# Performance work log

Measured on AMD Instinct MI355X. Metric: run time of the kernel, lower is better.

## Reference

```python
import jax, jax.numpy as jnp
import numpy as np
import math

B, T, C = 2, 2048, 1024
N_HEAD = 16
HEAD_DIM = C // N_HEAD


def setup_inputs() -> dict:
    key = jax.random.key(0)
    k1, k2, k3 = jax.random.split(key, 3)
    x = jax.random.normal(k1, (B, T, C), dtype=jnp.float32)
    # causal mask: positions where mask == 0 get -inf
    mask = jnp.tril(jnp.ones((T, T), dtype=bool))[None, None, :, :]
    W_attn = jax.random.normal(k2, (C, 3 * C), dtype=jnp.float32) * (1.0 / math.sqrt(C))
    b_attn = jnp.zeros((3 * C,), dtype=jnp.float32)
    W_proj = jax.random.normal(k3, (C, C), dtype=jnp.float32) * (1.0 / math.sqrt(C))
    b_proj = jnp.zeros((C,), dtype=jnp.float32)
    return {"x": x, "mask": mask, "W_attn": W_attn, "b_attn": b_attn,
            "W_proj": W_proj, "b_proj": b_proj}


def reference(x, mask, W_attn, b_attn, W_proj, b_proj):
    Bx, Tx, Cx = x.shape
    qkv = x @ W_attn + b_attn                      # [B,T,3C]
    q, k, v = jnp.split(qkv, 3, axis=2)
    # [B,T,C] -> [B,H,T,D]
    q = q.reshape(Bx, Tx, N_HEAD, HEAD_DIM).transpose(0, 2, 1, 3)
    k = k.reshape(Bx, Tx, N_HEAD, HEAD_DIM).transpose(0, 2, 1, 3)
    v = v.reshape(Bx, Tx, N_HEAD, HEAD_DIM).transpose(0, 2, 1, 3)
    scale = 1.0 / math.sqrt(HEAD_DIM)
    att = jnp.einsum('bhqd,bhkd->bhqk', q, k) * scale   # [B,H,T,T]
    att = jnp.where(mask, att, -jnp.inf)
    att = jax.nn.softmax(att, axis=-1)
    y = jnp.einsum('bhqk,bhkd->bhqd', att, v)            # [B,H,T,D]
    y = y.transpose(0, 2, 1, 3).reshape(Bx, Tx, Cx)      # [B,T,C]
    return y @ W_proj + b_proj
```

## Files before the change

### kernel.cpp

```cpp
#include <hip/hip_runtime.h>
#include <hip/hip_bf16.h>
#include <cstdint>

typedef unsigned short u16;
typedef unsigned int u32;
typedef unsigned long long u64;
using f32x4 = __attribute__((ext_vector_type(4))) float;
using s16x8 = __attribute__((ext_vector_type(8))) short;
using u32x4 = __attribute__((ext_vector_type(4))) u32;

#define NB 2
#define NT 2048
#define NC 1024
#define NH 16
#define HD 64

__device__ __forceinline__ u16 f2b(float f) {
    unsigned u = __float_as_uint(f);
    unsigned r = (u + 0x7FFFu + ((u >> 16) & 1u)) >> 16;
    return (u16)r;
}

__device__ __forceinline__ u32 cvtpk(float a, float b) {
    u32 r;
    asm("v_cvt_pk_bf16_f32 %0, %1, %2" : "=v"(r) : "v"(a), "v"(b));
    return r;
}
__device__ __forceinline__ void swap32(u32& a, u32& b) {
    asm("v_permlane32_swap_b32 %0, %1" : "+v"(a), "+v"(b));
}
__device__ __forceinline__ void swap16(u32& a, u32& b) {
    asm("v_permlane16_swap_b32 %0, %1" : "+v"(a), "+v"(b));
}

__device__ __forceinline__ void gl_lds16(const void* g, const void* l) {
    __builtin_amdgcn_global_load_lds(
        (const __attribute__((address_space(1))) unsigned int*)g,
        (__attribute__((address_space(3))) unsigned int*)l, 16, 0, 0);
}

__global__ __launch_bounds__(256) void conv_bf16(const float* __restrict__ in,
                                                 u16* __restrict__ out, int n4) {
    int i = blockIdx.x * 256 + threadIdx.x;
    if (i >= n4) return;
    float4 v = ((const float4*)in)[i];
    u64 pack = (u64)f2b(v.x) | ((u64)f2b(v.y) << 16) |
               ((u64)f2b(v.z) << 32) | ((u64)f2b(v.w) << 48);
    ((u64*)out)[i] = pack;
}

__global__ __launch_bounds__(256) void transpose_bf16(const float* __restrict__ W,
                                                      u16* __restrict__ Wt,
                                                      int K, int N) {
    __shared__ u16 s[64][65];
    const int n0 = blockIdx.x * 64, k0 = blockIdx.y * 64;
    const int t = threadIdx.x;
    const int tr = t >> 4, tc4 = (t & 15) * 4;
#pragma unroll
    for (int i = 0; i < 4; i++) {
        int r = tr + i * 16;
        float4 v = *(const float4*)&W[(size_t)(k0 + r) * N + n0 + tc4];
        s[r][tc4 + 0] = f2b(v.x);
        s[r][tc4 + 1] = f2b(v.y);
        s[r][tc4 + 2] = f2b(v.z);
        s[r][tc4 + 3] = f2b(v.w);
    }
    __syncthreads();
#pragma unroll
    for (int i = 0; i < 4; i++) {
        int nl = tr + i * 16;
        u64 pack = (u64)s[tc4 + 0][nl] | ((u64)s[tc4 + 1][nl] << 16) |
                   ((u64)s[tc4 + 2][nl] << 32) | ((u64)s[tc4 + 3][nl] << 48);
        *(u64*)&Wt[(size_t)(n0 + nl) * K + k0 + tc4] = pack;
    }
}

template <int OUT_BF16>
__global__ __launch_bounds__(256) void gemm_bt(const u16* __restrict__ A,
                                               const u16* __restrict__ Bt,
                                               const float* __restrict__ bias,
                                               void* __restrict__ Cout,
                                               int M, int N, int K) {
    __shared__ u16 As[2][128 * 32];
    __shared__ u16 Bs[2][128 * 32];
    const int tid = threadIdx.x;
    const int lane = tid & 63, w = tid >> 6;
    const int nx = gridDim.x;
    const int f = blockIdx.y * nx + blockIdx.x;
    const int qq = (nx * gridDim.y) >> 3;
    const int nid = (f & 7) * qq + (f >> 3);
    const int m0 = (nid / nx) * 128, n0 = (nid % nx) * 128;
    const int wm = w >> 1, wn = w & 1;
    f32x4 acc[4][4] = {};

    const int srow = 32 * w + (lane >> 2);
    const int scol = (lane & 3) * 8;
    const u16* aP0 = &A[(size_t)(m0 + srow) * K + scol];
    const u16* aP1 = aP0 + (size_t)16 * K;
    const u16* bP0 = &Bt[(size_t)(n0 + srow) * K + scol];
    const u16* bP1 = bP0 + (size_t)16 * K;

    auto STAGE = [&](int t) {
        const int buf = t & 1;
        const int k0 = t * 32;
        gl_lds16(aP0 + k0, &As[buf][w * 1024 + lane * 8]);
        gl_lds16(aP1 + k0, &As[buf][w * 1024 + 512 + lane * 8]);
        gl_lds16(bP0 + k0, &Bs[buf][w * 1024 + lane * 8]);
        gl_lds16(bP1 + k0, &Bs[buf][w * 1024 + 512 + lane * 8]);
    };

    const int nt = K >> 5;
    STAGE(0);
    for (int t = 0; t < nt; ++t) {
        asm volatile("s_waitcnt vmcnt(0)" ::: "memory");
        __builtin_amdgcn_s_barrier();
        if (t + 1 < nt) STAGE(t + 1);

        const u16* Asb = As[t & 1];
        const u16* Bsb = Bs[t & 1];
        s16x8 af[4], bf[4];
#pragma unroll
        for (int mt = 0; mt < 4; mt++)
            af[mt] = *(const s16x8*)&Asb[(wm * 64 + mt * 16 + (lane & 15)) * 32 + (lane >> 4) * 8];
#pragma unroll
        for (int nt2 = 0; nt2 < 4; nt2++)
            bf[nt2] = *(const s16x8*)&Bsb[(wn * 64 + nt2 * 16 + (lane & 15)) * 32 + (lane >> 4) * 8];
        __builtin_amdgcn_s_setprio(1);
#pragma unroll
        for (int mt = 0; mt < 4; mt++)
#pragma unroll
            for (int nt2 = 0; nt2 < 4; nt2++)
                acc[mt][nt2] = __builtin_amdgcn_mfma_f32_16x16x32_bf16(af[mt], bf[nt2], acc[mt][nt2], 0, 0, 0);
        __builtin_amdgcn_s_setprio(0);
    }

#pragma unroll
    for (int mt = 0; mt < 4; mt++) {
        int row = m0 + wm * 64 + mt * 16 + (lane >> 4) * 4;
#pragma unroll
        for (int nt2 = 0; nt2 < 4; nt2++) {
            int col = n0 + wn * 64 + nt2 * 16 + (lane & 15);
            float bs = bias[col];
#pragma unroll
            for (int r = 0; r < 4; r++) {
                float v = acc[mt][nt2][r] + bs;
                if (OUT_BF16)
                    ((u16*)Cout)[(size_t)(row + r) * N + col] = f2b(v);
                else
                    ((float*)Cout)[(size_t)(row + r) * N + col] = v;
            }
        }
    }
}

__global__ __launch_bounds__(256) void gemm_bt_n64(const u16* __restrict__ A,
                                                   const u16* __restrict__ Bt,
                                                   const float* __restrict__ bias,
                                                   float* __restrict__ Cout,
                                                   int M, int N, int K) {
    __shared__ u16 As[2][128 * 32];
    __shared__ u16 Bs[2][64 * 32];
    const int tid = threadIdx.x;
    const int lane = tid & 63, w = tid >> 6;
    const int nx = gridDim.x;
    const int f = blockIdx.y * nx + blockIdx.x;
    const int qq = (nx * gridDim.y) >> 3;
    const int nid = (f & 7) * qq + (f >> 3);
    const int m0 = (nid / nx) * 128, n0 = (nid % nx) * 64;
    f32x4 acc[2][4] = {};

    const int srow = 32 * w + (lane >> 2);
    const int srowB = 16 * w + (lane >> 2);
    const int scol = (lane & 3) * 8;
    const u16* aP0 = &A[(size_t)(m0 + srow) * K + scol];
    const u16* aP1 = aP0 + (size_t)16 * K;
    const u16* bP0 = &Bt[(size_t)(n0 + srowB) * K + scol];

    auto STAGE = [&](int t) {
        const int buf = t & 1;
        const int k0 = t * 32;
        gl_lds16(aP0 + k0, &As[buf][w * 1024 + lane * 8]);
        gl_lds16(aP1 + k0, &As[buf][w * 1024 + 512 + lane * 8]);
        gl_lds16(bP0 + k0, &Bs[buf][w * 512 + lane * 8]);
    };

    const int nt = K >> 5;
    STAGE(0);
    for (int t = 0; t < nt; ++t) {
        asm volatile("s_waitcnt vmcnt(0)" ::: "memory");
        __builtin_amdgcn_s_barrier();
        if (t + 1 < nt) STAGE(t + 1);

        const u16* Asb = As[t & 1];
        const u16* Bsb = Bs[t & 1];
        s16x8 af[2], bf[4];
#pragma unroll
        for (int mt = 0; mt < 2; mt++)
            af[mt] = *(const s16x8*)&Asb[(w * 32 + mt * 16 + (lane & 15)) * 32 + (lane >> 4) * 8];
#pragma unroll
        for (int nt2 = 0; nt2 < 4; nt2++)
            bf[nt2] = *(const s16x8*)&Bsb[(nt2 * 16 + (lane & 15)) * 32 + (lane >> 4) * 8];
        __builtin_amdgcn_s_setprio(1);
#pragma unroll
        for (int mt = 0; mt < 2; mt++)
#pragma unroll
            for (int nt2 = 0; nt2 < 4; nt2++)
                acc[mt][nt2] = __builtin_amdgcn_mfma_f32_16x16x32_bf16(af[mt], bf[nt2], acc[mt][nt2], 0, 0, 0);
        __builtin_amdgcn_s_setprio(0);
    }

#pragma unroll
    for (int mt = 0; mt < 2; mt++) {
        int row = m0 + w * 32 + mt * 16 + (lane >> 4) * 4;
#pragma unroll
        for (int nt2 = 0; nt2 < 4; nt2++) {
            int col = n0 + nt2 * 16 + (lane & 15);
            float bs = bias[col];
#pragma unroll
            for (int r = 0; r < 4; r++)
                Cout[(size_t)(row + r) * N + col] = acc[mt][nt2][r] + bs;
        }
    }
}

__global__ __launch_bounds__(256) void v_transpose(const u16* __restrict__ qkv,
                                                   u16* __restrict__ Vt) {
    __shared__ u16 s[64][65];
    const int t0 = blockIdx.x * 64;
    const int b = blockIdx.y >> 4, h = blockIdx.y & 15;
    const int t = threadIdx.x;
    const int tr = t >> 4, tc4 = (t & 15) * 4;
    const u16* src = qkv + (size_t)b * NT * (3 * NC) + 2 * NC + h * HD;
#pragma unroll
    for (int i = 0; i < 4; i++) {
        int r = tr + i * 16;
        u64 v = *(const u64*)&src[(size_t)(t0 + r) * (3 * NC) + tc4];
        s[r][tc4 + 0] = (u16)v;
        s[r][tc4 + 1] = (u16)(v >> 16);
        s[r][tc4 + 2] = (u16)(v >> 32);
        s[r][tc4 + 3] = (u16)(v >> 48);
    }
    __syncthreads();
    u16* dstb = Vt + (size_t)(b * NH + h) * HD * NT;
#pragma unroll
    for (int i = 0; i < 4; i++) {
        int d = tr + i * 16;
        u64 pack = (u64)s[tc4 + 0][d] | ((u64)s[tc4 + 1][d] << 16) |
                   ((u64)s[tc4 + 2][d] << 32) | ((u64)s[tc4 + 3][d] << 48);
        *(u64*)&dstb[(size_t)d * NT + t0 + tc4] = pack;
    }
}

__global__ __launch_bounds__(512) void attn_kernel(const u16* __restrict__ qkv,
                                                   const u16* __restrict__ Vt,
                                                   u16* __restrict__ yb) {
    __shared__ __align__(16) u16 Kb[2][2][64 * 64];
    __shared__ __align__(16) u16 Vb[2][2][64 * 64];

    const int l = threadIdx.x & 63;
    const int q16 = l & 15, g = l >> 4;
    const int wv = threadIdx.x >> 6;
    const int rg = wv & 3, hf = wv >> 2;
    const int i0 = blockIdx.x;
    const int xcd = i0 & 7, idx = i0 >> 3;
    const int hh = xcd * 4 + (idx >> 4);
    const int pr = idx & 15;
    const int b = hh >> 4, h = hh & 15;

    const u16* qkvb = qkv + (size_t)b * NT * (3 * NC);

    const int srow = l >> 3;
    const int sc8 = (l & 7) ^ (srow & 7);
    const u16* kSrc0 = qkvb + NC + h * HD + (size_t)(8 * rg + srow) * (3 * NC) + sc8 * 8;
    const u16* kSrc1 = kSrc0 + (size_t)32 * (3 * NC);
    const u16* vSrc0 = Vt + ((size_t)(b * NH + h) * HD + 8 * rg + srow) * NT + sc8 * 8;
    const u16* vSrc1 = vSrc0 + (size_t)32 * NT;
    const size_t kStep = (size_t)64 * (3 * NC);

    const float sc2 = 0.125f * 1.44269504088896340736f;
    const float SHIFT = 5.0f * 1.44269504088896340736f;
    const int sw = q16 & 7;

    u32 kfo[4][2], vfo[2][4];
#pragma unroll
    for (int ii = 0; ii < 4; ii++)
#pragma unroll
        for (int kc = 0; kc < 2; kc++)
            kfo[ii][kc] = (u32)(((16 * ii + q16) * 64 + ((4 * kc + g) ^ sw) * 8) * 2);
#pragma unroll
    for (int ks = 0; ks < 2; ks++)
#pragma unroll
        for (int dt = 0; dt < 4; dt++)
            vfo[ks][dt] = (u32)(((16 * dt + q16) * 64 + ((4 * ks + g) ^ sw) * 8) * 2);

#pragma unroll 1
    for (int sc = 0; sc < 2; ++sc) {
        const int cc = (sc == 0) ? (31 - pr) : pr;
        const int nt = cc + 1;
        const int h0 = (nt + 1) >> 1;
        const int base = hf ? h0 : 0;
        const int myN = hf ? (nt - h0) : h0;
        const int qw = cc * 64 + 16 * rg;

        s16x8 qf[2];
#pragma unroll
        for (int kc = 0; kc < 2; kc++)
            qf[kc] = *(const s16x8*)(qkvb + (size_t)(qw + q16) * (3 * NC) + h * HD + kc * 32 + g * 8);

        f32x4 yacc[4] = {};
        float lsum = 0.f;

        const u16* kP0 = kSrc0 + (size_t)base * kStep;
        const u16* kP1 = kSrc1 + (size_t)base * kStep;
        const u16* vP0 = vSrc0 + base * 64;
        const u16* vP1 = vSrc1 + base * 64;

        auto STAGE = [&](int buf) {
            gl_lds16(kP0, &Kb[hf][buf][rg * 512 + l * 8]);
            gl_lds16(kP1, &Kb[hf][buf][2048 + rg * 512 + l * 8]);
            gl_lds16(vP0, &Vb[hf][buf][rg * 512 + l * 8]);
            gl_lds16(vP1, &Vb[hf][buf][2048 + rg * 512 + l * 8]);
            kP0 += kStep; kP1 += kStep; vP0 += 64; vP1 += 64;
        };

        if (myN > 0) STAGE(base & 1);
        for (int u = 0; u < h0; ++u) {
            const int t = base + u;
            const bool act = (u < myN);
            asm volatile("s_waitcnt vmcnt(0)" ::: "memory");
            __builtin_amdgcn_s_barrier();
            if (u + 1 < myN) STAGE((t + 1) & 1);

            if (act) {
                const char* Kc = (const char*)&Kb[hf][t & 1][0];
                const char* Vc = (const char*)&Vb[hf][t & 1][0];

                s16x8 kf[4][2];
#pragma unroll
                for (int ii = 0; ii < 4; ii++)
#pragma unroll
                    for (int kc = 0; kc < 2; kc++)
                        kf[ii][kc] = *(const s16x8*)(Kc + kfo[ii][kc]);

                s16x8 vf0[4];
#pragma unroll
                for (int dt = 0; dt < 4; dt++)
                    vf0[dt] = *(const s16x8*)(Vc + vfo[0][dt]);

                f32x4 sacc[4] = {};
                __builtin_amdgcn_s_setprio(1);
#pragma unroll
                for (int ii = 0; ii < 4; ii++)
#pragma unroll
                    for (int kc = 0; kc < 2; kc++)
                        sacc[ii] = __builtin_amdgcn_mfma_f32_16x16x32_bf16(kf[ii][kc], qf[kc], sacc[ii], 0, 0, 0);
                __builtin_amdgcn_s_setprio(0);

                if (t == cc) {
                    const int kv0 = t * 64;
#pragma unroll
                    for (int ii = 0; ii < 4; ii++)
#pragma unroll
                        for (int r = 0; r < 4; r++)
                            if (kv0 + 16 * ii + 4 * g + r > qw + q16) sacc[ii][r] = -1e30f;
                }

                float p[4][4];
                float ps = 0.f;
#pragma unroll
                for (int ii = 0; ii < 4; ii++)
#pragma unroll
                    for (int r = 0; r < 4; r++) {
                        p[ii][r] = exp2f(fmaf(sacc[ii][r], sc2, -SHIFT));
                        ps += p[ii][r];
                    }
                lsum += ps;

                s16x8 pfrag[2];
#pragma unroll
                for (int ks = 0; ks < 2; ks++) {
                    u32 C0 = cvtpk(p[2 * ks][0], p[2 * ks][1]);
                    u32 C1 = cvtpk(p[2 * ks][2], p[2 * ks][3]);
                    u32 D0 = cvtpk(p[2 * ks + 1][0], p[2 * ks + 1][1]);
                    u32 D1 = cvtpk(p[2 * ks + 1][2], p[2 * ks + 1][3]);
                    swap32(C0, D0); swap16(C0, D0);
                    swap32(C1, D1); swap16(C1, D1);
                    u32x4 fr;
                    fr[0] = C0; fr[1] = C1; fr[2] = D0; fr[3] = D1;
                    pfrag[ks] = __builtin_bit_cast(s16x8, fr);
                }

                s16x8 vf1[4];
#pragma unroll
                for (int dt = 0; dt < 4; dt++)
                    vf1[dt] = *(const s16x8*)(Vc + vfo[1][dt]);

                __builtin_amdgcn_s_setprio(1);
#pragma unroll
                for (int dt = 0; dt < 4; dt++)
                    yacc[dt] = __builtin_amdgcn_mfma_f32_16x16x32_bf16(vf0[dt], pfrag[0], yacc[dt], 0, 0, 0);
#pragma unroll
                for (int dt = 0; dt < 4; dt++)
                    yacc[dt] = __builtin_amdgcn_mfma_f32_16x16x32_bf16(vf1[dt], pfrag[1], yacc[dt], 0, 0, 0);
                __builtin_amdgcn_s_setprio(0);
            }
        }
        __builtin_amdgcn_s_barrier();

        float* mY = (float*)&Kb[1][0][0];
        float* mL = (float*)&Vb[1][0][0];
        if (hf == 1) {
#pragma unroll
            for (int dt = 0; dt < 4; dt++)
#pragma unroll
                for (int r = 0; r < 4; r++)
                    mY[(rg * 16 + dt * 4 + r) * 64 + l] = yacc[dt][r];
            mL[rg * 64 + l] = lsum;
        }
        __syncthreads();
        if (hf == 0) {
#pragma unroll
            for (int dt = 0; dt < 4; dt++)
#pragma unroll
                for (int r = 0; r < 4; r++)
                    yacc[dt][r] += mY[(rg * 16 + dt * 4 + r) * 64 + l];
            lsum += mL[rg * 64 + l];
            lsum += __shfl_xor(lsum, 16);
            lsum += __shfl_xor(lsum, 32);
            float inv = 1.f / lsum;
            size_t rowoff = ((size_t)(b * NT + qw + q16)) * NC + h * HD;
#pragma unroll
            for (int dt = 0; dt < 4; dt++) {
                u32 lo = cvtpk(yacc[dt][0] * inv, yacc[dt][1] * inv);
                u32 hi = cvtpk(yacc[dt][2] * inv, yacc[dt][3] * inv);
                u64 pk = (u64)lo | ((u64)hi << 32);
                *(u64*)(yb + rowoff + 16 * dt + 4 * g) = pk;
            }
        }
        __syncthreads();
    }
}

extern "C" void kernel_launch(void* const* d_in, const int* in_sizes, int n_in,
                              void* d_out, int out_size, void* d_ws, size_t ws_size,
                              hipStream_t stream) {
    const float* x  = (const float*)d_in[0];
    const float* Wa = (const float*)d_in[2];
    const float* ba = (const float*)d_in[3];
    const float* Wp = (const float*)d_in[4];
    const float* bp = (const float*)d_in[5];
    float* out = (float*)d_out;

    char* ws = (char*)d_ws;
    u16* xb  = (u16*)(ws);
    u16* WaT = (u16*)(ws + (8ull << 20));
    u16* WpT = (u16*)(ws + (14ull << 20));
    u16* qkv = (u16*)(ws + (16ull << 20));
    u16* yb  = (u16*)(ws + (40ull << 20));
    u16* Vtb = (u16*)(ws + (48ull << 20));

    const int M = NB * NT;

    conv_bf16<<<(M * NC / 4 + 255) / 256, 256, 0, stream>>>(x, xb, M * NC / 4);
    transpose_bf16<<<dim3(3 * NC / 64, NC / 64), 256, 0, stream>>>(Wa, WaT, NC, 3 * NC);
    transpose_bf16<<<dim3(NC / 64, NC / 64), 256, 0, stream>>>(Wp, WpT, NC, NC);

    gemm_bt<1><<<dim3(3 * NC / 128, M / 128), 256, 0, stream>>>(xb, WaT, ba, qkv, M, 3 * NC, NC);

    v_transpose<<<dim3(NT / 64, NB * NH), 256, 0, stream>>>(qkv, Vtb);

    attn_kernel<<<dim3(NB * NH * 16), 512, 0, stream>>>(qkv, Vtb, yb);

    gemm_bt_n64<<<dim3(NC / 64, M / 128), 256, 0, stream>>>(yb, WpT, bp, out, M, NC, NC);
}
```

Baseline: 115.7 us.

## Merge prep kernels into one launch and fuse V transpose into QKV GEMM epilogue

The bf16 conversion of x and the two weight transposes now run as one combined prep kernel, which saves two launches. The QKV GEMM epilogue writes V tiles straight into a transposed layout through an LDS slab, so the separate v_transpose kernel and its extra read/write pass over V go away. In exchange the GEMM uses more LDS and gains two block-wide barriers in the V-tile epilogue. V is also no longer stored in the row-major qkv buffer.

```diff
diff --git a/kernel.cpp b/kernel.cpp
--- a/kernel.cpp
+++ b/kernel.cpp
@@ -39,22 +39,36 @@
         (__attribute__((address_space(3))) unsigned int*)l, 16, 0, 0);
 }
 
-__global__ __launch_bounds__(256) void conv_bf16(const float* __restrict__ in,
-                                                 u16* __restrict__ out, int n4) {
-    int i = blockIdx.x * 256 + threadIdx.x;
-    if (i >= n4) return;
-    float4 v = ((const float4*)in)[i];
-    u64 pack = (u64)f2b(v.x) | ((u64)f2b(v.y) << 16) |
-               ((u64)f2b(v.z) << 32) | ((u64)f2b(v.w) << 48);
-    ((u64*)out)[i] = pack;
-}
-
-__global__ __launch_bounds__(256) void transpose_bf16(const float* __restrict__ W,
-                                                      u16* __restrict__ Wt,
-                                                      int K, int N) {
+__global__ __launch_bounds__(256) void prep(const float* __restrict__ x,
+                                            u16* __restrict__ xb,
+                                            const float* __restrict__ Wa,
+                                            u16* __restrict__ WaT,
+                                            const float* __restrict__ Wp,
+                                            u16* __restrict__ WpT) {
     __shared__ u16 s[64][65];
-    const int n0 = blockIdx.x * 64, k0 = blockIdx.y * 64;
+    const int bid = blockIdx.x;
     const int t = threadIdx.x;
+
+    if (bid < 4096) {
+        int i = bid * 256 + t;
+        float4 v = ((const float4*)x)[i];
+        u64 pack = (u64)f2b(v.x) | ((u64)f2b(v.y) << 16) |
+                   ((u64)f2b(v.z) << 32) | ((u64)f2b(v.w) << 48);
+        ((u64*)xb)[i] = pack;
+        return;
+    }
+
+    const float* W; u16* Wt; int K, N, n0, k0;
+    if (bid < 4096 + 768) {
+        int q = bid - 4096;
+        W = Wa; Wt = WaT; K = 1024; N = 3072;
+        n0 = (q % 48) * 64; k0 = (q / 48) * 64;
+    } else {
+        int q = bid - 4096 - 768;
+        W = Wp; Wt = WpT; K = 1024; N = 1024;
+        n0 = (q % 16) * 64; k0 = (q / 16) * 64;
+    }
+
     const int tr = t >> 4, tc4 = (t & 15) * 4;
 #pragma unroll
     for (int i = 0; i < 4; i++) {
@@ -75,14 +89,15 @@
     }
 }
 
-template <int OUT_BF16>
-__global__ __launch_bounds__(256) void gemm_bt(const u16* __restrict__ A,
-                                               const u16* __restrict__ Bt,
-                                               const float* __restrict__ bias,
-                                               void* __restrict__ Cout,
-                                               int M, int N, int K) {
+__global__ __launch_bounds__(256) void gemm_qkv(const u16* __restrict__ A,
+                                                const u16* __restrict__ Bt,
+                                                const float* __restrict__ bias,
+                                                u16* __restrict__ Cout,
+                                                u16* __restrict__ Vt,
+                                                int M, int N, int K) {
     __shared__ u16 As[2][128 * 32];
     __shared__ u16 Bs[2][128 * 32];
+    __shared__ u16 slab[2][64][65];
     const int tid = threadIdx.x;
     const int lane = tid & 63, w = tid >> 6;
     const int nx = gridDim.x;
@@ -134,20 +149,51 @@
         __builtin_amdgcn_s_setprio(0);
     }
 
-#pragma unroll
-    for (int mt = 0; mt < 4; mt++) {
-        int row = m0 + wm * 64 + mt * 16 + (lane >> 4) * 4;
-#pragma unroll
-        for (int nt2 = 0; nt2 < 4; nt2++) {
-            int col = n0 + wn * 64 + nt2 * 16 + (lane & 15);
-            float bs = bias[col];
-#pragma unroll
-            for (int r = 0; r < 4; r++) {
-                float v = acc[mt][nt2][r] + bs;
-                if (OUT_BF16)
-                    ((u16*)Cout)[(size_t)(row + r) * N + col] = f2b(v);
-                else
-                    ((float*)Cout)[(size_t)(row + r) * N + col] = v;
+    if (n0 >= 2048) {
+        const int hG = ((n0 - 2048) >> 6) + wn;
+        const int bb = m0 >> 11;
+        const int tBase = (m0 & 2047) + wm * 64;
+        u16* vdst = Vt + ((size_t)(bb * NH + hG) * HD) * NT;
+#pragma unroll 1
+        for (int rd = 0; rd < 2; ++rd) {
+            if ((w >> 1) == rd) {
+                u16 (*sl)[65] = slab[w & 1];
+#pragma unroll
+                for (int mt = 0; mt < 4; mt++)
+#pragma unroll
+                    for (int nt2 = 0; nt2 < 4; nt2++) {
+                        int dl = nt2 * 16 + (lane & 15);
+                        float bs = bias[n0 + wn * 64 + dl];
+#pragma unroll
+                        for (int r = 0; r < 4; r++)
+                            sl[mt * 16 + (lane >> 4) * 4 + r][dl] = f2b(acc[mt][nt2][r] + bs);
+                    }
+            }
+            __syncthreads();
+            if ((w >> 1) == rd) {
+                u16 (*sl)[65] = slab[w & 1];
+#pragma unroll
+                for (int it = 0; it < 16; ++it) {
+                    int d = it * 4 + (lane >> 4);
+                    int tl4 = (lane & 15) * 4;
+                    u64 pk = (u64)sl[tl4 + 0][d] | ((u64)sl[tl4 + 1][d] << 16) |
+                             ((u64)sl[tl4 + 2][d] << 32) | ((u64)sl[tl4 + 3][d] << 48);
+                    *(u64*)&vdst[(size_t)d * NT + tBase + tl4] = pk;
+                }
+            }
+            __syncthreads();
+        }
+    } else {
+#pragma unroll
+        for (int mt = 0; mt < 4; mt++) {
+            int row = m0 + wm * 64 + mt * 16 + (lane >> 4) * 4;
+#pragma unroll
+            for (int nt2 = 0; nt2 < 4; nt2++) {
+                int col = n0 + wn * 64 + nt2 * 16 + (lane & 15);
+                float bs = bias[col];
+#pragma unroll
+                for (int r = 0; r < 4; r++)
+                    Cout[(size_t)(row + r) * N + col] = f2b(acc[mt][nt2][r] + bs);
             }
         }
     }
@@ -223,34 +269,6 @@
     }
 }
 
-__global__ __launch_bounds__(256) void v_transpose(const u16* __restrict__ qkv,
-                                                   u16* __restrict__ Vt) {
-    __shared__ u16 s[64][65];
-    const int t0 = blockIdx.x * 64;
-    const int b = blockIdx.y >> 4, h = blockIdx.y & 15;
-    const int t = threadIdx.x;
-    const int tr = t >> 4, tc4 = (t & 15) * 4;
-    const u16* src = qkv + (size_t)b * NT * (3 * NC) + 2 * NC + h * HD;
-#pragma unroll
-    for (int i = 0; i < 4; i++) {
-        int r = tr + i * 16;
-        u64 v = *(const u64*)&src[(size_t)(t0 + r) * (3 * NC) + tc4];
-        s[r][tc4 + 0] = (u16)v;
-        s[r][tc4 + 1] = (u16)(v >> 16);
-        s[r][tc4 + 2] = (u16)(v >> 32);
-        s[r][tc4 + 3] = (u16)(v >> 48);
-    }
-    __syncthreads();
-    u16* dstb = Vt + (size_t)(b * NH + h) * HD * NT;
-#pragma unroll
-    for (int i = 0; i < 4; i++) {
-        int d = tr + i * 16;
-        u64 pack = (u64)s[tc4 + 0][d] | ((u64)s[tc4 + 1][d] << 16) |
-                   ((u64)s[tc4 + 2][d] << 32) | ((u64)s[tc4 + 3][d] << 48);
-        *(u64*)&dstb[(size_t)d * NT + t0 + tc4] = pack;
-    }
-}
-
 __global__ __launch_bounds__(512) void attn_kernel(const u16* __restrict__ qkv,
                                                    const u16* __restrict__ Vt,
                                                    u16* __restrict__ yb) {
@@ -461,13 +479,9 @@
 
     const int M = NB * NT;
 
-    conv_bf16<<<(M * NC / 4 + 255) / 256, 256, 0, stream>>>(x, xb, M * NC / 4);
-    transpose_bf16<<<dim3(3 * NC / 64, NC / 64), 256, 0, stream>>>(Wa, WaT, NC, 3 * NC);
-    transpose_bf16<<<dim3(NC / 64, NC / 64), 256, 0, stream>>>(Wp, WpT, NC, NC);
-
-    gemm_bt<1><<<dim3(3 * NC / 128, M / 128), 256, 0, stream>>>(xb, WaT, ba, qkv, M, 3 * NC, NC);
-
-    v_transpose<<<dim3(NT / 64, NB * NH), 256, 0, stream>>>(qkv, Vtb);
+    prep<<<dim3(4096 + 768 + 256), 256, 0, stream>>>(x, xb, Wa, WaT, Wp, WpT);
+
+    gemm_qkv<<<dim3(3 * NC / 128, M / 128), 256, 0, stream>>>(xb, WaT, ba, qkv, Vtb, M, 3 * NC, NC);
 
     attn_kernel<<<dim3(NB * NH * 16), 512, 0, stream>>>(qkv, Vtb, yb);
 
```

New measurement: 121.4 us. 4.9% more time.

## Merge prep kernels into one launch and XOR-swizzle GEMM LDS chunks

Applied to the files above, without the earlier changes.

The input conversion and both weight transposes now run in a single kernel that dispatches on block index, removing two kernel launches and their gaps. Both GEMM kernels also XOR-swizzle the 16-byte chunk column on the global-to-LDS load and apply the matching swizzle on the LDS fragment reads, to cut LDS bank conflicts. The combined kernel hardcodes problem sizes in its block-range split, and the swizzle has to stay consistent between writer and reader lanes to remain correct.

```diff
diff --git a/kernel.cpp b/kernel.cpp
--- a/kernel.cpp
+++ b/kernel.cpp
@@ -39,22 +39,36 @@
         (__attribute__((address_space(3))) unsigned int*)l, 16, 0, 0);
 }
 
-__global__ __launch_bounds__(256) void conv_bf16(const float* __restrict__ in,
-                                                 u16* __restrict__ out, int n4) {
-    int i = blockIdx.x * 256 + threadIdx.x;
-    if (i >= n4) return;
-    float4 v = ((const float4*)in)[i];
-    u64 pack = (u64)f2b(v.x) | ((u64)f2b(v.y) << 16) |
-               ((u64)f2b(v.z) << 32) | ((u64)f2b(v.w) << 48);
-    ((u64*)out)[i] = pack;
-}
-
-__global__ __launch_bounds__(256) void transpose_bf16(const float* __restrict__ W,
-                                                      u16* __restrict__ Wt,
-                                                      int K, int N) {
+__global__ __launch_bounds__(256) void prep(const float* __restrict__ x,
+                                            u16* __restrict__ xb,
+                                            const float* __restrict__ Wa,
+                                            u16* __restrict__ WaT,
+                                            const float* __restrict__ Wp,
+                                            u16* __restrict__ WpT) {
     __shared__ u16 s[64][65];
-    const int n0 = blockIdx.x * 64, k0 = blockIdx.y * 64;
+    const int bid = blockIdx.x;
     const int t = threadIdx.x;
+
+    if (bid < 4096) {
+        int i = bid * 256 + t;
+        float4 v = ((const float4*)x)[i];
+        u64 pack = (u64)f2b(v.x) | ((u64)f2b(v.y) << 16) |
+                   ((u64)f2b(v.z) << 32) | ((u64)f2b(v.w) << 48);
+        ((u64*)xb)[i] = pack;
+        return;
+    }
+
+    const float* W; u16* Wt; int K, N, n0, k0;
+    if (bid < 4096 + 768) {
+        int q = bid - 4096;
+        W = Wa; Wt = WaT; K = 1024; N = 3072;
+        n0 = (q % 48) * 64; k0 = (q / 48) * 64;
+    } else {
+        int q = bid - 4096 - 768;
+        W = Wp; Wt = WpT; K = 1024; N = 1024;
+        n0 = (q % 16) * 64; k0 = (q / 16) * 64;
+    }
+
     const int tr = t >> 4, tc4 = (t & 15) * 4;
 #pragma unroll
     for (int i = 0; i < 4; i++) {
@@ -94,7 +108,7 @@
     f32x4 acc[4][4] = {};
 
     const int srow = 32 * w + (lane >> 2);
-    const int scol = (lane & 3) * 8;
+    const int scol = (((lane & 3) ^ ((lane >> 2) & 3)) * 8);
     const u16* aP0 = &A[(size_t)(m0 + srow) * K + scol];
     const u16* aP1 = aP0 + (size_t)16 * K;
     const u16* bP0 = &Bt[(size_t)(n0 + srow) * K + scol];
@@ -109,6 +123,8 @@
         gl_lds16(bP1 + k0, &Bs[buf][w * 1024 + 512 + lane * 8]);
     };
 
+    const int rchunk = (((lane >> 4) ^ (lane & 3)) * 8);
+
     const int nt = K >> 5;
     STAGE(0);
     for (int t = 0; t < nt; ++t) {
@@ -121,10 +137,10 @@
         s16x8 af[4], bf[4];
 #pragma unroll
         for (int mt = 0; mt < 4; mt++)
-            af[mt] = *(const s16x8*)&Asb[(wm * 64 + mt * 16 + (lane & 15)) * 32 + (lane >> 4) * 8];
+            af[mt] = *(const s16x8*)&Asb[(wm * 64 + mt * 16 + (lane & 15)) * 32 + rchunk];
 #pragma unroll
         for (int nt2 = 0; nt2 < 4; nt2++)
-            bf[nt2] = *(const s16x8*)&Bsb[(wn * 64 + nt2 * 16 + (lane & 15)) * 32 + (lane >> 4) * 8];
+            bf[nt2] = *(const s16x8*)&Bsb[(wn * 64 + nt2 * 16 + (lane & 15)) * 32 + rchunk];
         __builtin_amdgcn_s_setprio(1);
 #pragma unroll
         for (int mt = 0; mt < 4; mt++)
@@ -171,7 +187,7 @@
 
     const int srow = 32 * w + (lane >> 2);
     const int srowB = 16 * w + (lane >> 2);
-    const int scol = (lane & 3) * 8;
+    const int scol = (((lane & 3) ^ ((lane >> 2) & 3)) * 8);
     const u16* aP0 = &A[(size_t)(m0 + srow) * K + scol];
     const u16* aP1 = aP0 + (size_t)16 * K;
     const u16* bP0 = &Bt[(size_t)(n0 + srowB) * K + scol];
@@ -184,6 +200,8 @@
         gl_lds16(bP0 + k0, &Bs[buf][w * 512 + lane * 8]);
     };
 
+    const int rchunk = (((lane >> 4) ^ (lane & 3)) * 8);
+
     const int nt = K >> 5;
     STAGE(0);
     for (int t = 0; t < nt; ++t) {
@@ -196,10 +214,10 @@
         s16x8 af[2], bf[4];
 #pragma unroll
         for (int mt = 0; mt < 2; mt++)
-            af[mt] = *(const s16x8*)&Asb[(w * 32 + mt * 16 + (lane & 15)) * 32 + (lane >> 4) * 8];
+            af[mt] = *(const s16x8*)&Asb[(w * 32 + mt * 16 + (lane & 15)) * 32 + rchunk];
 #pragma unroll
         for (int nt2 = 0; nt2 < 4; nt2++)
-            bf[nt2] = *(const s16x8*)&Bsb[(nt2 * 16 + (lane & 15)) * 32 + (lane >> 4) * 8];
+            bf[nt2] = *(const s16x8*)&Bsb[(nt2 * 16 + (lane & 15)) * 32 + rchunk];
         __builtin_amdgcn_s_setprio(1);
 #pragma unroll
         for (int mt = 0; mt < 2; mt++)
@@ -461,9 +479,7 @@
 
     const int M = NB * NT;
 
-    conv_bf16<<<(M * NC / 4 + 255) / 256, 256, 0, stream>>>(x, xb, M * NC / 4);
-    transpose_bf16<<<dim3(3 * NC / 64, NC / 64), 256, 0, stream>>>(Wa, WaT, NC, 3 * NC);
-    transpose_bf16<<<dim3(NC / 64, NC / 64), 256, 0, stream>>>(Wp, WpT, NC, NC);
+    prep<<<dim3(4096 + 768 + 256), 256, 0, stream>>>(x, xb, Wa, WaT, Wp, WpT);
 
     gemm_bt<1><<<dim3(3 * NC / 128, M / 128), 256, 0, stream>>>(xb, WaT, ba, qkv, M, 3 * NC, NC);
 
```

Measured after the change: 114.4 us (median of 2 runs). No clear change (-1.1%).
